# Performance work log

Hardware: AMD Instinct MI355X
Metric: run time of the kernel (lower is better)

The kernel has to match this reference:

```python
import jax, jax.numpy as jnp
import numpy as np

N_NODES = 100000
N_EDGES = 1600000
IN_DIM = 128
HID = 128
OUT = 128
NUM_GRAPHS = 2048


def setup_inputs() -> dict:
    key = jax.random.key(0)
    ks = jax.random.split(key, 10)
    x = jax.random.normal(ks[0], (N_NODES, IN_DIM), dtype=jnp.float32)
    edge_index = jax.random.randint(ks[1], (2, N_EDGES), 0, N_NODES, dtype=jnp.int32)
    graph_index = jnp.sort(jax.random.randint(ks[2], (N_NODES,), 0, NUM_GRAPHS, dtype=jnp.int32))
    def glorot(k, fi, fo):
        lim = jnp.sqrt(6.0 / (fi + fo)).astype(jnp.float32)
        return jax.random.uniform(k, (fi, fo), jnp.float32, -lim, lim)
    return {
        "x": x,
        "edge_index": edge_index,
        "graph_index": graph_index,
        "num_graphs": NUM_GRAPHS,
        "W1": glorot(ks[3], IN_DIM, HID), "b1": jnp.zeros((HID,), jnp.float32),
        "W2": glorot(ks[4], HID, HID),    "b2": jnp.zeros((HID,), jnp.float32),
        "W3": glorot(ks[5], HID, OUT),    "b3": jnp.zeros((OUT,), jnp.float32),
    }


def _gcn_layer(x, src, dst, norm, W, b, n_nodes):
    # transform first (cheap GEMM), then normalized gather-scatter aggregation
    h = x @ W                              # [N, F]
    msg = h[src] * norm[:, None]           # [E+N, F] gather + scale
    out = jax.ops.segment_sum(msg, dst, num_segments=n_nodes)  # scatter-add
    return out + b


def reference(x, edge_index, graph_index, num_graphs, W1, b1, W2, b2, W3, b3):
    n = x.shape[0]
    # add self-loops (PyG GCNConv default)
    loops = jnp.arange(n, dtype=edge_index.dtype)
    src = jnp.concatenate([edge_index[0], loops])
    dst = jnp.concatenate([edge_index[1], loops])
    # symmetric normalization D^-1/2 (A+I) D^-1/2, degree = in-degree incl. self-loop
    deg = jax.ops.segment_sum(jnp.ones_like(src, dtype=x.dtype), dst, num_segments=n)
    dinv = jax.lax.rsqrt(jnp.maximum(deg, 1.0))
    norm = dinv[src] * dinv[dst]
    # 3 conv layers + ReLU (dropout = identity at inference)
    h = jax.nn.relu(_gcn_layer(x, src, dst, norm, W1, b1, n))
    h = jax.nn.relu(_gcn_layer(h, src, dst, norm, W2, b2, n))
    h = jax.nn.relu(_gcn_layer(h, src, dst, norm, W3, b3, n))
    # global mean / max pooling per graph
    gsum = jax.ops.segment_sum(h, graph_index, num_segments=num_graphs)
    cnt = jax.ops.segment_sum(jnp.ones((n,), h.dtype), graph_index, num_segments=num_graphs)
    gmean = gsum / jnp.maximum(cnt, 1.0)[:, None]
    gmax = jax.ops.segment_max(h, graph_index, num_segments=num_graphs)
    return jnp.concatenate([gmean, gmax], axis=-1)
```

## Files before the change

### kernel.cpp

```cpp
#include <hip/hip_runtime.h>
#include <hip/hip_bf16.h>
#include <stdint.h>

#define N_NODES   100000
#define N_EDGES   1600000
#define FDIM      128
#define NUM_GR    2048
#define CSR_CAP   64

#define NBKT      391
#define BKT_CAP   4864
#define TILE      4096
#define LBIN_CAP  16
#define LBIN_STR  17

typedef __attribute__((ext_vector_type(8))) short short8;
typedef __attribute__((ext_vector_type(4))) float f32x4;

__device__ __forceinline__ uint32_t pk2(float a, float b) {
    __hip_bfloat16 x = __float2bfloat16(a), y = __float2bfloat16(b);
    uint16_t ux = *reinterpret_cast<uint16_t*>(&x);
    uint16_t uy = *reinterpret_cast<uint16_t*>(&y);
    return (uint32_t)ux | ((uint32_t)uy << 16);
}

__device__ __forceinline__ float bflo(uint32_t u) { return __uint_as_float(u << 16); }
__device__ __forceinline__ float bfhi(uint32_t u) { return __uint_as_float(u & 0xFFFF0000u); }

__device__ __forceinline__ short8 pack8(float4 u0, float4 u1) {
    union { uint32_t u[4]; short8 s; } cv;
    cv.u[0] = pk2(u0.x, u0.y);
    cv.u[1] = pk2(u0.z, u0.w);
    cv.u[2] = pk2(u1.x, u1.y);
    cv.u[3] = pk2(u1.z, u1.w);
    return cv.s;
}

__device__ __forceinline__ int lower_bound_dev(const int* a, int n, int key) {
    int lo = 0, hi = n;
    while (lo < hi) {
        int m = (lo + hi) >> 1;
        if (a[m] < key) lo = m + 1; else hi = m;
    }
    return lo;
}


__global__ __launch_bounds__(256, 4) void k_fused1(
        const float* __restrict__ x, const float* __restrict__ W1,
        __hip_bfloat16* __restrict__ C, int n, int gGemm,
        const int* __restrict__ src, const int* __restrict__ dst,
        int* __restrict__ bkt_cnt, int* __restrict__ bkt, int E, int gA,
        const float* __restrict__ W2, const float* __restrict__ W3,
        __hip_bfloat16* __restrict__ wt,
        const int* __restrict__ gidx, float* __restrict__ gscale) {
    __shared__ uint32_t smem[8192];
    const int b = blockIdx.x;
    const int tid = threadIdx.x;

    if (b >= gGemm + gA + 128) {
        int g = (b - (gGemm + gA + 128)) * 256 + tid;
        if (g < NUM_GR) {
            int lo = lower_bound_dev(gidx, n, g);
            int hi = lower_bound_dev(gidx, n, g + 1);
            gscale[g] = 1.f / (float)max(hi - lo, 1);
        }
        return;
    }

    if (b >= gGemm + gA) {
        int idx = 16384 + (b - gGemm - gA) * 256 + tid;
        int l = idx >> 14, rem = idx & 16383, c = rem >> 7, k = rem & 127;
        const float* W = (l == 1) ? W2 : W3;
        wt[idx] = __float2bfloat16(W[k * FDIM + c]);
        return;
    }

    if (b >= gGemm) {
        int* binCnt  = (int*)smem;
        int* binBase = (int*)smem + NBKT;
        int* bins    = (int*)smem + 2 * NBKT;
        int bb = b - gGemm;

        for (int i = tid; i < NBKT; i += 256) binCnt[i] = 0;
        __syncthreads();

        int e0 = bb * TILE;
        int e1 = min(E, e0 + TILE);
        for (int e = e0 + tid; e < e1; e += 256) {
            int s = src[e];
            int d = dst[e];
            int bi = d >> 8;
            int rec = ((d & 255) << 17) | s;
            int pos = atomicAdd(&binCnt[bi], 1);
            if (pos < LBIN_CAP) {
                bins[bi * LBIN_STR + pos] = rec;
            } else {
                int gp = atomicAdd(&bkt_cnt[bi], 1);
                if (gp < BKT_CAP) bkt[bi * BKT_CAP + gp] = rec;
            }
        }
        __syncthreads();

        for (int i = tid; i < NBKT; i += 256) {
            int c = min(binCnt[i], LBIN_CAP);
            binBase[i] = (c > 0) ? atomicAdd(&bkt_cnt[i], c) : 0;
        }
        __syncthreads();

        for (int i = tid; i < NBKT * LBIN_CAP; i += 256) {
            int bi = i / LBIN_CAP, sl = i - bi * LBIN_CAP;
            if (sl < min(binCnt[bi], LBIN_CAP)) {
                int gp = binBase[bi] + sl;
                if (gp < BKT_CAP) bkt[bi * BKT_CAP + gp] = bins[bi * LBIN_STR + sl];
            }
        }
        return;
    }

    uint32_t* Wtl = smem;

    const int rowBase = b * 128;

    for (int it = 0; it < 32; ++it) {
        int idx = it * 256 + tid;
        int kp = idx >> 7;
        int c  = idx & 127;
        float w0 = W1[(size_t)(2 * kp) * FDIM + c];
        float w1 = W1[(size_t)(2 * kp + 1) * FDIM + c];
        int word = c * 64 + ((((kp >> 2) ^ (c & 7)) << 2) | (kp & 3));
        Wtl[word] = pk2(w0, w1);
    }
    __syncthreads();

    const int w = tid >> 6;
    const int lane = tid & 63;
    const int r = lane & 15;
    const int q = lane >> 4;

    const int r0c = min(rowBase + w * 32 + r, n - 1);
    const int r1c = min(rowBase + w * 32 + 16 + r, n - 1);

    f32x4 acc[8][2] = {};

#pragma unroll
    for (int kk = 0; kk < 4; ++kk) {
        int co = (kk * 4 + q) * 8;
        const float4* p0 = (const float4*)&x[(size_t)r0c * FDIM + co];
        const float4* p1 = (const float4*)&x[(size_t)r1c * FDIM + co];
        short8 a0 = pack8(p0[0], p0[1]);
        short8 a1 = pack8(p1[0], p1[1]);
        int gr = ((kk * 4 + q) ^ (r & 7)) << 2;
#pragma unroll
        for (int m = 0; m < 8; ++m) {
            short8 bw = *(const short8*)&Wtl[(m * 16 + r) * 64 + gr];
            acc[m][0] = __builtin_amdgcn_mfma_f32_16x16x32_bf16(bw, a0, acc[m][0], 0, 0, 0);
            acc[m][1] = __builtin_amdgcn_mfma_f32_16x16x32_bf16(bw, a1, acc[m][1], 0, 0, 0);
        }
    }

#pragma unroll
    for (int nt = 0; nt < 2; ++nt) {
        int node = rowBase + w * 32 + nt * 16 + r;
        if (node < n) {
#pragma unroll
            for (int m = 0; m < 8; ++m) {
                f32x4 v = acc[m][nt];
                uint2 pv;
                pv.x = pk2(v[0], v[1]);
                pv.y = pk2(v[2], v[3]);
                *(uint2*)&C[(size_t)node * FDIM + m * 16 + q * 4] = pv;
            }
        }
    }
}


__global__ __launch_bounds__(256) void k_csr(const int* __restrict__ bkt_cnt,
                                             const int* __restrict__ bkt,
                                             int* __restrict__ cnt,
                                             float* __restrict__ dinv,
                                             int* __restrict__ csr, int n) {
    __shared__ int lc[64];
    __shared__ int cur[64];
    int b = blockIdx.x;
    int tid = threadIdx.x;
    int bi = b >> 2;
    int qd = b & 3;

    if (b == 0 && tid == 0) dinv[n] = 0.f;

    if (tid < 64) { lc[tid] = 0; cur[tid] = 0; }
    __syncthreads();

    int len = min(bkt_cnt[bi], BKT_CAP);
    const int* recs = bkt + bi * BKT_CAP;

    for (int i = tid; i < len; i += 256) {
        int dl = (recs[i] >> 17) & 255;
        if ((dl >> 6) == qd) atomicAdd(&lc[dl & 63], 1);
    }
    __syncthreads();

    if (tid < 64) {
        int v = (bi << 8) + (qd << 6) + tid;
        if (v < n) {
            int c = lc[tid];
            cnt[v] = c;
            dinv[v] = rsqrtf((float)(c + 1));
        }
    }

    for (int i = tid; i < len; i += 256) {
        int rec = recs[i];
        int dl = (rec >> 17) & 255;
        if ((dl >> 6) == qd) {
            int pos = atomicAdd(&cur[dl & 63], 1);
            if (pos < CSR_CAP)
                csr[(((size_t)(bi << 8) + dl) << 6) + pos] = rec & 0x1FFFF;
        }
    }
}


__global__ __launch_bounds__(256, 4) void k_gemm(const __hip_bfloat16* __restrict__ Ap,
                                                 const __hip_bfloat16* __restrict__ Wt,
                                                 const float* __restrict__ dinv,
                                                 __hip_bfloat16* __restrict__ C, int n) {
    __shared__ uint32_t Wtl[128 * 64];

    const int tid = threadIdx.x;
    const int rowBase = blockIdx.x * 128;

    for (int it = 0; it < 8; ++it) {
        int g = it * 256 + tid;
        int r = g >> 4;
        int seg = g & 15;
        uint4 v = *(const uint4*)&Wt[(size_t)r * FDIM + seg * 8];
        int word = r * 64 + ((seg ^ (r & 7)) << 2);
        *(uint4*)&Wtl[word] = v;
    }
    __syncthreads();

    const int w = tid >> 6;
    const int lane = tid & 63;
    const int r = lane & 15;
    const int q = lane >> 4;

    const uint4* A4 = (const uint4*)Ap;
    const int r0c = min(rowBase + w * 32 + r, n - 1);
    const int r1c = min(rowBase + w * 32 + 16 + r, n - 1);

    f32x4 acc[8][2] = {};

#pragma unroll
    for (int kk = 0; kk < 4; ++kk) {
        short8 a0 = *(const short8*)&A4[(size_t)r0c * 16 + kk * 4 + q];
        short8 a1 = *(const short8*)&A4[(size_t)r1c * 16 + kk * 4 + q];
        int gr = ((kk * 4 + q) ^ (r & 7)) << 2;
#pragma unroll
        for (int m = 0; m < 8; ++m) {
            short8 bw = *(const short8*)&Wtl[(m * 16 + r) * 64 + gr];
            acc[m][0] = __builtin_amdgcn_mfma_f32_16x16x32_bf16(bw, a0, acc[m][0], 0, 0, 0);
            acc[m][1] = __builtin_amdgcn_mfma_f32_16x16x32_bf16(bw, a1, acc[m][1], 0, 0, 0);
        }
    }

#pragma unroll
    for (int nt = 0; nt < 2; ++nt) {
        int node = rowBase + w * 32 + nt * 16 + r;
        if (node < n) {
            float dv = dinv[node];
#pragma unroll
            for (int m = 0; m < 8; ++m) {
                f32x4 v = acc[m][nt];
                uint2 pv;
                pv.x = pk2(v[0] * dv, v[1] * dv);
                pv.y = pk2(v[2] * dv, v[3] * dv);
                *(uint2*)&C[(size_t)node * FDIM + m * 16 + q * 4] = pv;
            }
        }
    }
}


template<int WEIGHTED, int POOL>
__global__ __launch_bounds__(256) void k_agg(const __hip_bfloat16* __restrict__ T,
                                             const int* __restrict__ cnt,
                                             const int* __restrict__ csr,
                                             const float* __restrict__ dinv,
                                             const float* __restrict__ bias,
                                             uint32_t* __restrict__ Hb,
                                             const int* __restrict__ gidx,
                                             const float* __restrict__ gscale,
                                             float* __restrict__ out,
                                             int n) {
    int wid = (blockIdx.x * 256 + threadIdx.x) >> 6;
    int lane = threadIdx.x & 63;
    if (wid >= n) return;
    int v = wid;
    int g   = lane >> 4;
    int s16 = lane & 15;

    const uint4* Tu4 = (const uint4*)T;

    int cv  = min(cnt[v], CSR_CAP);
    int sraw = csr[((size_t)v << 6) + lane];
    int sidx = (lane < cv) ? sraw : ((lane == cv) ? v : n);
    cv += 1;

    float a0 = 0.f, a1 = 0.f, a2 = 0.f, a3 = 0.f;
    float a4 = 0.f, a5 = 0.f, a6 = 0.f, a7 = 0.f;

    int mr = (cv + 15) & ~15;
    for (int j = 0; j < mr; j += 16) {
        uint4 gg[4];
        float wv[4];
#pragma unroll
        for (int t = 0; t < 4; ++t) {
            int it = __shfl(sidx, j + 4 * t + g, 64);
            if constexpr (WEIGHTED) wv[t] = dinv[it];
            gg[t] = Tu4[(size_t)it * 16 + s16];
        }
#pragma unroll
        for (int t = 0; t < 4; ++t) {
            if constexpr (WEIGHTED) {
                a0 = fmaf(wv[t], bflo(gg[t].x), a0); a1 = fmaf(wv[t], bfhi(gg[t].x), a1);
                a2 = fmaf(wv[t], bflo(gg[t].y), a2); a3 = fmaf(wv[t], bfhi(gg[t].y), a3);
                a4 = fmaf(wv[t], bflo(gg[t].z), a4); a5 = fmaf(wv[t], bfhi(gg[t].z), a5);
                a6 = fmaf(wv[t], bflo(gg[t].w), a6); a7 = fmaf(wv[t], bfhi(gg[t].w), a7);
            } else {
                a0 += bflo(gg[t].x); a1 += bfhi(gg[t].x);
                a2 += bflo(gg[t].y); a3 += bfhi(gg[t].y);
                a4 += bflo(gg[t].z); a5 += bfhi(gg[t].z);
                a6 += bflo(gg[t].w); a7 += bfhi(gg[t].w);
            }
        }
    }

    a0 += __shfl_xor(a0, 16, 64); a0 += __shfl_xor(a0, 32, 64);
    a1 += __shfl_xor(a1, 16, 64); a1 += __shfl_xor(a1, 32, 64);
    a2 += __shfl_xor(a2, 16, 64); a2 += __shfl_xor(a2, 32, 64);
    a3 += __shfl_xor(a3, 16, 64); a3 += __shfl_xor(a3, 32, 64);
    a4 += __shfl_xor(a4, 16, 64); a4 += __shfl_xor(a4, 32, 64);
    a5 += __shfl_xor(a5, 16, 64); a5 += __shfl_xor(a5, 32, 64);
    a6 += __shfl_xor(a6, 16, 64); a6 += __shfl_xor(a6, 32, 64);
    a7 += __shfl_xor(a7, 16, 64); a7 += __shfl_xor(a7, 32, 64);

    if constexpr (!POOL) {
        if (g == 0) {
            float dv = dinv[v];
            float4 bb0 = *(const float4*)&bias[s16 * 8];
            float4 bb1 = *(const float4*)&bias[s16 * 8 + 4];
            float r0 = fmaxf(fmaf(dv, a0, bb0.x), 0.f);
            float r1 = fmaxf(fmaf(dv, a1, bb0.y), 0.f);
            float r2 = fmaxf(fmaf(dv, a2, bb0.z), 0.f);
            float r3 = fmaxf(fmaf(dv, a3, bb0.w), 0.f);
            float r4 = fmaxf(fmaf(dv, a4, bb1.x), 0.f);
            float r5 = fmaxf(fmaf(dv, a5, bb1.y), 0.f);
            float r6 = fmaxf(fmaf(dv, a6, bb1.z), 0.f);
            float r7 = fmaxf(fmaf(dv, a7, bb1.w), 0.f);
            uint4 pv;
            pv.x = pk2(r0, r1);
            pv.y = pk2(r2, r3);
            pv.z = pk2(r4, r5);
            pv.w = pk2(r6, r7);
            *(uint4*)&Hb[(size_t)v * 64 + s16 * 4] = pv;
        }
    } else {
        __shared__ float lds_h[4 * 128];
        __shared__ int   lds_g[4];
        int wave = threadIdx.x >> 6;
        if (g == 0) {
            float dv = dinv[v];
            float4 bb0 = *(const float4*)&bias[s16 * 8];
            float4 bb1 = *(const float4*)&bias[s16 * 8 + 4];
            float* hh = &lds_h[wave * 128 + s16 * 8];
            hh[0] = fmaxf(fmaf(dv, a0, bb0.x), 0.f);
            hh[1] = fmaxf(fmaf(dv, a1, bb0.y), 0.f);
            hh[2] = fmaxf(fmaf(dv, a2, bb0.z), 0.f);
            hh[3] = fmaxf(fmaf(dv, a3, bb0.w), 0.f);
            hh[4] = fmaxf(fmaf(dv, a4, bb1.x), 0.f);
            hh[5] = fmaxf(fmaf(dv, a5, bb1.y), 0.f);
            hh[6] = fmaxf(fmaf(dv, a6, bb1.z), 0.f);
            hh[7] = fmaxf(fmaf(dv, a7, bb1.w), 0.f);
            if (s16 == 0) lds_g[wave] = gidx[v];
        }
        __syncthreads();
        if (threadIdx.x < 128) {
            int f = threadIdx.x;
            int cg = lds_g[0];
            float s = 0.f, m = 0.f;
#pragma unroll
            for (int ww = 0; ww < 4; ++ww) {
                int gw = lds_g[ww];
                float hv = lds_h[ww * 128 + f];
                if (gw != cg) {
                    atomicAdd(&out[(size_t)cg * 256 + f], s * gscale[cg]);
                    atomicMax((unsigned int*)&out[(size_t)cg * 256 + 128 + f],
                              __float_as_uint(m));
                    s = 0.f; m = 0.f; cg = gw;
                }
                s += hv;
                m = fmaxf(m, hv);
            }
            atomicAdd(&out[(size_t)cg * 256 + f], s * gscale[cg]);
            atomicMax((unsigned int*)&out[(size_t)cg * 256 + 128 + f],
                      __float_as_uint(m));
        }
    }
}


extern "C" void kernel_launch(void* const* d_in, const int* in_sizes, int n_in,
                              void* d_out, int out_size, void* d_ws, size_t ws_size,
                              hipStream_t stream) {
    const float* x    = (const float*)d_in[0];
    const int*   ei   = (const int*)d_in[1];
    const int*   gidx = (const int*)d_in[2];
    const float* W1 = (const float*)d_in[4];
    const float* b1 = (const float*)d_in[5];
    const float* W2 = (const float*)d_in[6];
    const float* b2 = (const float*)d_in[7];
    const float* W3 = (const float*)d_in[8];
    const float* b3 = (const float*)d_in[9];
    float* out = (float*)d_out;

    const int N = N_NODES, E = N_EDGES;
    const int* src = ei;
    const int* dst = ei + E;

    char* ws = (char*)d_ws;
    size_t o = 0;
    auto alloc = [&](size_t bytes) { size_t r = o; o += (bytes + 255) & ~(size_t)255; return r; };
    size_t o_bktcnt = alloc((size_t)NBKT * 4);
    size_t o_bkt    = alloc((size_t)NBKT * BKT_CAP * 4);
    size_t o_cnt    = alloc((size_t)N * 4);
    size_t o_dinv   = alloc((size_t)(N + 1) * 4);
    size_t o_csr    = alloc((size_t)NBKT * 256 * CSR_CAP * 4);
    size_t o_wt     = alloc((size_t)3 * FDIM * FDIM * 2);
    size_t o_t      = alloc((size_t)(N + 1) * FDIM * 2);
    size_t o_h      = alloc((size_t)N * FDIM * 2);
    size_t o_gs     = alloc((size_t)NUM_GR * 4);

    int*   bkt_cnt = (int*)(ws + o_bktcnt);
    int*   bkt     = (int*)(ws + o_bkt);
    int*   cnt     = (int*)(ws + o_cnt);
    float* dinv    = (float*)(ws + o_dinv);
    int*   csr     = (int*)(ws + o_csr);
    __hip_bfloat16* wtbuf = (__hip_bfloat16*)(ws + o_wt);
    __hip_bfloat16* tbuf  = (__hip_bfloat16*)(ws + o_t);
    __hip_bfloat16* hb16  = (__hip_bfloat16*)(ws + o_h);
    float* gscale = (float*)(ws + o_gs);

    hipMemsetAsync(bkt_cnt, 0, (size_t)NBKT * 4, stream);
    hipMemsetAsync(tbuf + (size_t)N * FDIM, 0, FDIM * 2, stream);
    hipMemsetAsync(out, 0, (size_t)NUM_GR * 2 * FDIM * 4, stream);

    const int gA    = (E + TILE - 1) / TILE;
    const int gGemm = (N + 127) / 128;

    k_fused1<<<gGemm + gA + 128 + 8, 256, 0, stream>>>(x, W1, tbuf, N, gGemm,
                                                       src, dst, bkt_cnt, bkt, E, gA,
                                                       W2, W3, wtbuf, gidx, gscale);
    k_csr<<<NBKT * 4, 256, 0, stream>>>(bkt_cnt, bkt, cnt, dinv, csr, N);

    const int gAgg = (N + 3) / 4;

    k_agg<1, 0><<<gAgg, 256, 0, stream>>>(tbuf, cnt, csr, dinv, b1, (uint32_t*)hb16,
                                          nullptr, nullptr, nullptr, N);
    k_gemm<<<gGemm, 256, 0, stream>>>(hb16, wtbuf + FDIM * FDIM, dinv, tbuf, N);
    k_agg<0, 0><<<gAgg, 256, 0, stream>>>(tbuf, cnt, csr, dinv, b2, (uint32_t*)hb16,
                                          nullptr, nullptr, nullptr, N);
    k_gemm<<<gGemm, 256, 0, stream>>>(hb16, wtbuf + 2 * FDIM * FDIM, dinv, tbuf, N);
    k_agg<0, 1><<<gAgg, 256, 0, stream>>>(tbuf, cnt, csr, dinv, b3, nullptr,
                                          gidx, gscale, out, N);
}
```

Baseline: 381.1 us.

## Fuse aggregation with following GEMM for layers two and three

Layers two and three now aggregate first and then multiply by the weight, using an A(HW) = (AH)W reordering. Each 512-thread block gathers 32 node rows into shared memory and runs an MFMA against a shared-memory copy of the weight, then applies bias/ReLU or pooling. This drops the separate GEMM kernels and the round trip of the intermediate activation through global memory. In exchange every block reloads the 32 KB weight, the gather now reads un-prescaled rows with a per-neighbour dinv weight, and the grid of N/32 assumes N is divisible by 32.

```diff
diff --git a/kernel.cpp b/kernel.cpp
--- a/kernel.cpp
+++ b/kernel.cpp
@@ -223,78 +223,13 @@
 }
 
 
-__global__ __launch_bounds__(256, 4) void k_gemm(const __hip_bfloat16* __restrict__ Ap,
-                                                 const __hip_bfloat16* __restrict__ Wt,
-                                                 const float* __restrict__ dinv,
-                                                 __hip_bfloat16* __restrict__ C, int n) {
-    __shared__ uint32_t Wtl[128 * 64];
-
-    const int tid = threadIdx.x;
-    const int rowBase = blockIdx.x * 128;
-
-    for (int it = 0; it < 8; ++it) {
-        int g = it * 256 + tid;
-        int r = g >> 4;
-        int seg = g & 15;
-        uint4 v = *(const uint4*)&Wt[(size_t)r * FDIM + seg * 8];
-        int word = r * 64 + ((seg ^ (r & 7)) << 2);
-        *(uint4*)&Wtl[word] = v;
-    }
-    __syncthreads();
-
-    const int w = tid >> 6;
-    const int lane = tid & 63;
-    const int r = lane & 15;
-    const int q = lane >> 4;
-
-    const uint4* A4 = (const uint4*)Ap;
-    const int r0c = min(rowBase + w * 32 + r, n - 1);
-    const int r1c = min(rowBase + w * 32 + 16 + r, n - 1);
-
-    f32x4 acc[8][2] = {};
-
-#pragma unroll
-    for (int kk = 0; kk < 4; ++kk) {
-        short8 a0 = *(const short8*)&A4[(size_t)r0c * 16 + kk * 4 + q];
-        short8 a1 = *(const short8*)&A4[(size_t)r1c * 16 + kk * 4 + q];
-        int gr = ((kk * 4 + q) ^ (r & 7)) << 2;
-#pragma unroll
-        for (int m = 0; m < 8; ++m) {
-            short8 bw = *(const short8*)&Wtl[(m * 16 + r) * 64 + gr];
-            acc[m][0] = __builtin_amdgcn_mfma_f32_16x16x32_bf16(bw, a0, acc[m][0], 0, 0, 0);
-            acc[m][1] = __builtin_amdgcn_mfma_f32_16x16x32_bf16(bw, a1, acc[m][1], 0, 0, 0);
-        }
-    }
-
-#pragma unroll
-    for (int nt = 0; nt < 2; ++nt) {
-        int node = rowBase + w * 32 + nt * 16 + r;
-        if (node < n) {
-            float dv = dinv[node];
-#pragma unroll
-            for (int m = 0; m < 8; ++m) {
-                f32x4 v = acc[m][nt];
-                uint2 pv;
-                pv.x = pk2(v[0] * dv, v[1] * dv);
-                pv.y = pk2(v[2] * dv, v[3] * dv);
-                *(uint2*)&C[(size_t)node * FDIM + m * 16 + q * 4] = pv;
-            }
-        }
-    }
-}
-
-
-template<int WEIGHTED, int POOL>
-__global__ __launch_bounds__(256) void k_agg(const __hip_bfloat16* __restrict__ T,
-                                             const int* __restrict__ cnt,
-                                             const int* __restrict__ csr,
-                                             const float* __restrict__ dinv,
-                                             const float* __restrict__ bias,
-                                             uint32_t* __restrict__ Hb,
-                                             const int* __restrict__ gidx,
-                                             const float* __restrict__ gscale,
-                                             float* __restrict__ out,
-                                             int n) {
+__global__ __launch_bounds__(256) void k_agg1(const __hip_bfloat16* __restrict__ T,
+                                              const int* __restrict__ cnt,
+                                              const int* __restrict__ csr,
+                                              const float* __restrict__ dinv,
+                                              const float* __restrict__ bias,
+                                              uint32_t* __restrict__ Hb,
+                                              int n) {
     int wid = (blockIdx.x * 256 + threadIdx.x) >> 6;
     int lane = threadIdx.x & 63;
     if (wid >= n) return;
@@ -319,22 +254,15 @@
 #pragma unroll
         for (int t = 0; t < 4; ++t) {
             int it = __shfl(sidx, j + 4 * t + g, 64);
-            if constexpr (WEIGHTED) wv[t] = dinv[it];
+            wv[t] = dinv[it];
             gg[t] = Tu4[(size_t)it * 16 + s16];
         }
 #pragma unroll
         for (int t = 0; t < 4; ++t) {
-            if constexpr (WEIGHTED) {
-                a0 = fmaf(wv[t], bflo(gg[t].x), a0); a1 = fmaf(wv[t], bfhi(gg[t].x), a1);
-                a2 = fmaf(wv[t], bflo(gg[t].y), a2); a3 = fmaf(wv[t], bfhi(gg[t].y), a3);
-                a4 = fmaf(wv[t], bflo(gg[t].z), a4); a5 = fmaf(wv[t], bfhi(gg[t].z), a5);
-                a6 = fmaf(wv[t], bflo(gg[t].w), a6); a7 = fmaf(wv[t], bfhi(gg[t].w), a7);
-            } else {
-                a0 += bflo(gg[t].x); a1 += bfhi(gg[t].x);
-                a2 += bflo(gg[t].y); a3 += bfhi(gg[t].y);
-                a4 += bflo(gg[t].z); a5 += bfhi(gg[t].z);
-                a6 += bflo(gg[t].w); a7 += bfhi(gg[t].w);
-            }
+            a0 = fmaf(wv[t], bflo(gg[t].x), a0); a1 = fmaf(wv[t], bfhi(gg[t].x), a1);
+            a2 = fmaf(wv[t], bflo(gg[t].y), a2); a3 = fmaf(wv[t], bfhi(gg[t].y), a3);
+            a4 = fmaf(wv[t], bflo(gg[t].z), a4); a5 = fmaf(wv[t], bfhi(gg[t].z), a5);
+            a6 = fmaf(wv[t], bflo(gg[t].w), a6); a7 = fmaf(wv[t], bfhi(gg[t].w), a7);
         }
     }
 
@@ -347,54 +275,166 @@
     a6 += __shfl_xor(a6, 16, 64); a6 += __shfl_xor(a6, 32, 64);
     a7 += __shfl_xor(a7, 16, 64); a7 += __shfl_xor(a7, 32, 64);
 
-    if constexpr (!POOL) {
+    if (g == 0) {
+        float dv = dinv[v];
+        float4 bb0 = *(const float4*)&bias[s16 * 8];
+        float4 bb1 = *(const float4*)&bias[s16 * 8 + 4];
+        float r0 = fmaxf(fmaf(dv, a0, bb0.x), 0.f);
+        float r1 = fmaxf(fmaf(dv, a1, bb0.y), 0.f);
+        float r2 = fmaxf(fmaf(dv, a2, bb0.z), 0.f);
+        float r3 = fmaxf(fmaf(dv, a3, bb0.w), 0.f);
+        float r4 = fmaxf(fmaf(dv, a4, bb1.x), 0.f);
+        float r5 = fmaxf(fmaf(dv, a5, bb1.y), 0.f);
+        float r6 = fmaxf(fmaf(dv, a6, bb1.z), 0.f);
+        float r7 = fmaxf(fmaf(dv, a7, bb1.w), 0.f);
+        uint4 pv;
+        pv.x = pk2(r0, r1);
+        pv.y = pk2(r2, r3);
+        pv.z = pk2(r4, r5);
+        pv.w = pk2(r6, r7);
+        *(uint4*)&Hb[(size_t)v * 64 + s16 * 4] = pv;
+    }
+}
+
+
+template<int POOL>
+__global__ __launch_bounds__(512, 4) void k_aggT(
+        const __hip_bfloat16* __restrict__ T,
+        const __hip_bfloat16* __restrict__ Wt,
+        const int* __restrict__ cnt,
+        const int* __restrict__ csr,
+        const float* __restrict__ dinv,
+        const float* __restrict__ bias,
+        uint32_t* __restrict__ Hb,
+        const int* __restrict__ gidx,
+        const float* __restrict__ gscale,
+        float* __restrict__ out,
+        int n) {
+    __shared__ uint32_t Wl[128 * 64];
+    __shared__ uint32_t Hl[32 * 64];
+
+    const int tid = threadIdx.x;
+
+    for (int it = 0; it < 4; ++it) {
+        int g = it * 512 + tid;
+        int r = g >> 4;
+        int seg = g & 15;
+        uint4 v = *(const uint4*)&Wt[(size_t)r * FDIM + seg * 8];
+        int word = r * 64 + ((seg ^ (r & 7)) << 2);
+        *(uint4*)&Wl[word] = v;
+    }
+
+    const int w = tid >> 6;
+    const int lane = tid & 63;
+    const int g = lane >> 4;
+    const int s16 = lane & 15;
+    const int nodeBase = blockIdx.x * 32;
+    const uint4* Tu4 = (const uint4*)T;
+
+    for (int k = 0; k < 4; ++k) {
+        int v = nodeBase + w * 4 + k;
+        int cv = min(cnt[v], CSR_CAP);
+        int sraw = csr[((size_t)v << 6) + lane];
+        int sidx = (lane < cv) ? sraw : ((lane == cv) ? v : n);
+        cv += 1;
+
+        float a0 = 0.f, a1 = 0.f, a2 = 0.f, a3 = 0.f;
+        float a4 = 0.f, a5 = 0.f, a6 = 0.f, a7 = 0.f;
+
+        int mr = (cv + 15) & ~15;
+        for (int j = 0; j < mr; j += 16) {
+            uint4 gg[4];
+            float wv[4];
+#pragma unroll
+            for (int t = 0; t < 4; ++t) {
+                int it = __shfl(sidx, j + 4 * t + g, 64);
+                wv[t] = dinv[it];
+                gg[t] = Tu4[(size_t)it * 16 + s16];
+            }
+#pragma unroll
+            for (int t = 0; t < 4; ++t) {
+                a0 = fmaf(wv[t], bflo(gg[t].x), a0); a1 = fmaf(wv[t], bfhi(gg[t].x), a1);
+                a2 = fmaf(wv[t], bflo(gg[t].y), a2); a3 = fmaf(wv[t], bfhi(gg[t].y), a3);
+                a4 = fmaf(wv[t], bflo(gg[t].z), a4); a5 = fmaf(wv[t], bfhi(gg[t].z), a5);
+                a6 = fmaf(wv[t], bflo(gg[t].w), a6); a7 = fmaf(wv[t], bfhi(gg[t].w), a7);
+            }
+        }
+
+        a0 += __shfl_xor(a0, 16, 64); a0 += __shfl_xor(a0, 32, 64);
+        a1 += __shfl_xor(a1, 16, 64); a1 += __shfl_xor(a1, 32, 64);
+        a2 += __shfl_xor(a2, 16, 64); a2 += __shfl_xor(a2, 32, 64);
+        a3 += __shfl_xor(a3, 16, 64); a3 += __shfl_xor(a3, 32, 64);
+        a4 += __shfl_xor(a4, 16, 64); a4 += __shfl_xor(a4, 32, 64);
+        a5 += __shfl_xor(a5, 16, 64); a5 += __shfl_xor(a5, 32, 64);
+        a6 += __shfl_xor(a6, 16, 64); a6 += __shfl_xor(a6, 32, 64);
+        a7 += __shfl_xor(a7, 16, 64); a7 += __shfl_xor(a7, 32, 64);
+
         if (g == 0) {
             float dv = dinv[v];
-            float4 bb0 = *(const float4*)&bias[s16 * 8];
-            float4 bb1 = *(const float4*)&bias[s16 * 8 + 4];
-            float r0 = fmaxf(fmaf(dv, a0, bb0.x), 0.f);
-            float r1 = fmaxf(fmaf(dv, a1, bb0.y), 0.f);
-            float r2 = fmaxf(fmaf(dv, a2, bb0.z), 0.f);
-            float r3 = fmaxf(fmaf(dv, a3, bb0.w), 0.f);
-            float r4 = fmaxf(fmaf(dv, a4, bb1.x), 0.f);
-            float r5 = fmaxf(fmaf(dv, a5, bb1.y), 0.f);
-            float r6 = fmaxf(fmaf(dv, a6, bb1.z), 0.f);
-            float r7 = fmaxf(fmaf(dv, a7, bb1.w), 0.f);
+            int row = w * 4 + k;
             uint4 pv;
+            pv.x = pk2(a0 * dv, a1 * dv);
+            pv.y = pk2(a2 * dv, a3 * dv);
+            pv.z = pk2(a4 * dv, a5 * dv);
+            pv.w = pk2(a6 * dv, a7 * dv);
+            *(uint4*)&Hl[row * 64 + ((s16 ^ (row & 7)) << 2)] = pv;
+        }
+    }
+    __syncthreads();
+
+    const int r = lane & 15;
+    const int q = lane >> 4;
+
+    f32x4 acc[2] = {};
+#pragma unroll
+    for (int kk = 0; kk < 4; ++kk) {
+        int gr = ((kk * 4 + q) ^ (r & 7)) << 2;
+        short8 a0 = *(const short8*)&Hl[r * 64 + gr];
+        short8 a1 = *(const short8*)&Hl[(16 + r) * 64 + gr];
+        short8 bw = *(const short8*)&Wl[(w * 16 + r) * 64 + gr];
+        acc[0] = __builtin_amdgcn_mfma_f32_16x16x32_bf16(bw, a0, acc[0], 0, 0, 0);
+        acc[1] = __builtin_amdgcn_mfma_f32_16x16x32_bf16(bw, a1, acc[1], 0, 0, 0);
+    }
+
+    float4 bb = *(const float4*)&bias[w * 16 + q * 4];
+
+    if constexpr (!POOL) {
+#pragma unroll
+        for (int nt = 0; nt < 2; ++nt) {
+            int node = nodeBase + nt * 16 + r;
+            f32x4 vv = acc[nt];
+            float r0 = fmaxf(vv[0] + bb.x, 0.f);
+            float r1 = fmaxf(vv[1] + bb.y, 0.f);
+            float r2 = fmaxf(vv[2] + bb.z, 0.f);
+            float r3 = fmaxf(vv[3] + bb.w, 0.f);
+            uint2 pv;
             pv.x = pk2(r0, r1);
             pv.y = pk2(r2, r3);
-            pv.z = pk2(r4, r5);
-            pv.w = pk2(r6, r7);
-            *(uint4*)&Hb[(size_t)v * 64 + s16 * 4] = pv;
+            *(uint2*)&Hb[(size_t)node * 64 + w * 8 + q * 2] = pv;
         }
     } else {
-        __shared__ float lds_h[4 * 128];
-        __shared__ int   lds_g[4];
-        int wave = threadIdx.x >> 6;
-        if (g == 0) {
-            float dv = dinv[v];
-            float4 bb0 = *(const float4*)&bias[s16 * 8];
-            float4 bb1 = *(const float4*)&bias[s16 * 8 + 4];
-            float* hh = &lds_h[wave * 128 + s16 * 8];
-            hh[0] = fmaxf(fmaf(dv, a0, bb0.x), 0.f);
-            hh[1] = fmaxf(fmaf(dv, a1, bb0.y), 0.f);
-            hh[2] = fmaxf(fmaf(dv, a2, bb0.z), 0.f);
-            hh[3] = fmaxf(fmaf(dv, a3, bb0.w), 0.f);
-            hh[4] = fmaxf(fmaf(dv, a4, bb1.x), 0.f);
-            hh[5] = fmaxf(fmaf(dv, a5, bb1.y), 0.f);
-            hh[6] = fmaxf(fmaf(dv, a6, bb1.z), 0.f);
-            hh[7] = fmaxf(fmaf(dv, a7, bb1.w), 0.f);
-            if (s16 == 0) lds_g[wave] = gidx[v];
-        }
         __syncthreads();
-        if (threadIdx.x < 128) {
-            int f = threadIdx.x;
+        float* Pl = (float*)Wl;
+        int* lds_g = (int*)Hl;
+#pragma unroll
+        for (int nt = 0; nt < 2; ++nt) {
+            int row = nt * 16 + r;
+            f32x4 vv = acc[nt];
+            float* dstp = &Pl[row * 130 + w * 16 + q * 4];
+            dstp[0] = fmaxf(vv[0] + bb.x, 0.f);
+            dstp[1] = fmaxf(vv[1] + bb.y, 0.f);
+            dstp[2] = fmaxf(vv[2] + bb.z, 0.f);
+            dstp[3] = fmaxf(vv[3] + bb.w, 0.f);
+        }
+        if (tid < 32) lds_g[tid] = gidx[nodeBase + tid];
+        __syncthreads();
+        if (tid < 128) {
+            int f = tid;
             int cg = lds_g[0];
             float s = 0.f, m = 0.f;
-#pragma unroll
-            for (int ww = 0; ww < 4; ++ww) {
-                int gw = lds_g[ww];
-                float hv = lds_h[ww * 128 + f];
+            for (int row = 0; row < 32; ++row) {
+                int gw = lds_g[row];
+                float hv = Pl[row * 130 + f];
                 if (gw != cg) {
                     atomicAdd(&out[(size_t)cg * 256 + f], s * gscale[cg]);
                     atomicMax((unsigned int*)&out[(size_t)cg * 256 + 128 + f],
@@ -439,8 +479,8 @@
     size_t o_dinv   = alloc((size_t)(N + 1) * 4);
     size_t o_csr    = alloc((size_t)NBKT * 256 * CSR_CAP * 4);
     size_t o_wt     = alloc((size_t)3 * FDIM * FDIM * 2);
-    size_t o_t      = alloc((size_t)(N + 1) * FDIM * 2);
-    size_t o_h      = alloc((size_t)N * FDIM * 2);
+    size_t o_ta     = alloc((size_t)(N + 1) * FDIM * 2);
+    size_t o_tb     = alloc((size_t)(N + 1) * FDIM * 2);
     size_t o_gs     = alloc((size_t)NUM_GR * 4);
 
     int*   bkt_cnt = (int*)(ws + o_bktcnt);
@@ -449,30 +489,29 @@
     float* dinv    = (float*)(ws + o_dinv);
     int*   csr     = (int*)(ws + o_csr);
     __hip_bfloat16* wtbuf = (__hip_bfloat16*)(ws + o_wt);
-    __hip_bfloat16* tbuf  = (__hip_bfloat16*)(ws + o_t);
-    __hip_bfloat16* hb16  = (__hip_bfloat16*)(ws + o_h);
+    __hip_bfloat16* bufA  = (__hip_bfloat16*)(ws + o_ta);
+    __hip_bfloat16* bufB  = (__hip_bfloat16*)(ws + o_tb);
     float* gscale = (float*)(ws + o_gs);
 
     hipMemsetAsync(bkt_cnt, 0, (size_t)NBKT * 4, stream);
-    hipMemsetAsync(tbuf + (size_t)N * FDIM, 0, FDIM * 2, stream);
+    hipMemsetAsync(bufA + (size_t)N * FDIM, 0, FDIM * 2, stream);
+    hipMemsetAsync(bufB + (size_t)N * FDIM, 0, FDIM * 2, stream);
     hipMemsetAsync(out, 0, (size_t)NUM_GR * 2 * FDIM * 4, stream);
 
     const int gA    = (E + TILE - 1) / TILE;
     const int gGemm = (N + 127) / 128;
 
-    k_fused1<<<gGemm + gA + 128 + 8, 256, 0, stream>>>(x, W1, tbuf, N, gGemm,
+    k_fused1<<<gGemm + gA + 128 + 8, 256, 0, stream>>>(x, W1, bufA, N, gGemm,
                                                        src, dst, bkt_cnt, bkt, E, gA,
                                                        W2, W3, wtbuf, gidx, gscale);
     k_csr<<<NBKT * 4, 256, 0, stream>>>(bkt_cnt, bkt, cnt, dinv, csr, N);
 
-    const int gAgg = (N + 3) / 4;
-
-    k_agg<1, 0><<<gAgg, 256, 0, stream>>>(tbuf, cnt, csr, dinv, b1, (uint32_t*)hb16,
+    k_agg1<<<(N + 3) / 4, 256, 0, stream>>>(bufA, cnt, csr, dinv, b1,
+                                            (uint32_t*)bufB, N);
+    k_aggT<0><<<N / 32, 512, 0, stream>>>(bufB, wtbuf + FDIM * FDIM,
+                                          cnt, csr, dinv, b2, (uint32_t*)bufA,
                                           nullptr, nullptr, nullptr, N);
-    k_gemm<<<gGemm, 256, 0, stream>>>(hb16, wtbuf + FDIM * FDIM, dinv, tbuf, N);
-    k_agg<0, 0><<<gAgg, 256, 0, stream>>>(tbuf, cnt, csr, dinv, b2, (uint32_t*)hb16,
-                                          nullptr, nullptr, nullptr, N);
-    k_gemm<<<gGemm, 256, 0, stream>>>(hb16, wtbuf + 2 * FDIM * FDIM, dinv, tbuf, N);
-    k_agg<0, 1><<<gAgg, 256, 0, stream>>>(tbuf, cnt, csr, dinv, b3, nullptr,
+    k_aggT<1><<<N / 32, 512, 0, stream>>>(bufA, wtbuf + 2 * FDIM * FDIM,
+                                          cnt, csr, dinv, b3, nullptr,
                                           gidx, gscale, out, N);
 }
```

Result: faster. 368.6 us (-3.3%).
